# Optimization experiments

Hardware: AMD Instinct MI355X
Metric: run time of the kernel (lower is better)

Reference implementation:

```python
import jax, jax.numpy as jnp
import numpy as np

B, C, H, Wd = 4, 64, 64, 64


def setup_inputs() -> dict:
    key = jax.random.key(0)
    k1, k2, k3 = jax.random.split(key, 3)
    x = jax.random.normal(k1, (B, C, H, Wd), dtype=jnp.float32)
    W = jax.random.normal(k2, (C, C), dtype=jnp.float32) * (1.0 / np.sqrt(C))
    b = jax.random.normal(k3, (C,), dtype=jnp.float32) * 0.01
    return {"x": x, "W": W, "b": b}


def reference(x, W, b):
    Bz, Cz, Hz, Wz = x.shape
    N = Hz * Wz
    xf = x.reshape(Bz, Cz, N)                      # values [B,C,N]
    # shared 1x1 conv for queries and keys (same module instance in torch)
    qk = jnp.einsum('oc,bcn->bon', W, xf) + b[None, :, None]  # [B,C,N]
    # scores[b,n,m] = sum_c q[b,c,n] * k[b,c,m], scaled by 1/N
    scores = jnp.einsum('bcn,bcm->bnm', qk, qk) / N           # [B,N,N]
    attn = jax.nn.softmax(scores, axis=-1)                    # softmax over m
    # out[b,c,n] = sum_m values[b,c,m] * attn[b,n,m]
    out = jnp.einsum('bcm,bnm->bcn', xf, attn)
    return out.reshape(Bz, Cz, Hz, Wz)
```

## Files before the change

### kernel.cpp

```cpp
#include <hip/hip_runtime.h>
#include <hip/hip_bf16.h>

#define BATCH 4
#define NSP   4096

typedef __bf16 bf16x8v __attribute__((ext_vector_type(8)));
typedef __bf16 bf16x4v __attribute__((ext_vector_type(4)));
typedef float  floatx4 __attribute__((ext_vector_type(4)));

__global__ __launch_bounds__(256) void qk_kernel(const float* __restrict__ x,
                                                 const float* __restrict__ Wm,
                                                 const float* __restrict__ bias,
                                                 __bf16* __restrict__ qkT) {
    __shared__ __align__(16) __bf16 xT[64 * 72];

    const int t  = threadIdx.x;
    const int b  = blockIdx.x >> 6;
    const int n0 = (blockIdx.x & 63) << 6;

#pragma unroll
    for (int p = 0; p < 4; ++p) {
        const int c  = p * 16 + (t >> 4);
        const int n4 = (t & 15) * 4;
        const float4 v = *(const float4*)(x + (size_t)(b * 64 + c) * 4096 + n0 + n4);
        xT[(n4 + 0) * 72 + c] = (__bf16)(v.x * 0.015625f);
        xT[(n4 + 1) * 72 + c] = (__bf16)(v.y * 0.015625f);
        xT[(n4 + 2) * 72 + c] = (__bf16)(v.z * 0.015625f);
        xT[(n4 + 3) * 72 + c] = (__bf16)(v.w * 0.015625f);
    }
    __syncthreads();

    const int w = t >> 6, lane = t & 63, quad = lane >> 4, l16 = lane & 15;
    const bf16x8v a0 = *(const bf16x8v*)(xT + (w * 16 + l16) * 72 + quad * 8);
    const bf16x8v a1 = *(const bf16x8v*)(xT + (w * 16 + l16) * 72 + 32 + quad * 8);

    floatx4 acc[4];
#pragma unroll
    for (int ot = 0; ot < 4; ++ot) {
        const float* wr = Wm + (ot * 16 + l16) * 64;
        float4 wa = *(const float4*)(wr + quad * 8);
        float4 wb = *(const float4*)(wr + quad * 8 + 4);
        float4 wc = *(const float4*)(wr + 32 + quad * 8);
        float4 wd = *(const float4*)(wr + 32 + quad * 8 + 4);
        bf16x8v b0, b1;
        b0[0]=(__bf16)wa.x; b0[1]=(__bf16)wa.y; b0[2]=(__bf16)wa.z; b0[3]=(__bf16)wa.w;
        b0[4]=(__bf16)wb.x; b0[5]=(__bf16)wb.y; b0[6]=(__bf16)wb.z; b0[7]=(__bf16)wb.w;
        b1[0]=(__bf16)wc.x; b1[1]=(__bf16)wc.y; b1[2]=(__bf16)wc.z; b1[3]=(__bf16)wc.w;
        b1[4]=(__bf16)wd.x; b1[5]=(__bf16)wd.y; b1[6]=(__bf16)wd.z; b1[7]=(__bf16)wd.w;
        acc[ot] = floatx4{0.f, 0.f, 0.f, 0.f};
        acc[ot] = __builtin_amdgcn_mfma_f32_16x16x32_bf16(a0, b0, acc[ot], 0, 0, 0);
        acc[ot] = __builtin_amdgcn_mfma_f32_16x16x32_bf16(a1, b1, acc[ot], 0, 0, 0);
    }
    __syncthreads();

#pragma unroll
    for (int ot = 0; ot < 4; ++ot) {
        const float bo = bias[ot * 16 + l16] * 0.015625f;
#pragma unroll
        for (int r = 0; r < 4; ++r)
            xT[(w * 16 + quad * 4 + r) * 72 + ot * 16 + l16] = (__bf16)(acc[ot][r] + bo);
    }
    __syncthreads();

    const int n = t >> 2, seg = t & 3;
    __bf16* dst = qkT + (size_t)(b * 4096 + n0 + n) * 64 + seg * 16;
    *(bf16x8v*)dst       = *(const bf16x8v*)(xT + n * 72 + seg * 16);
    *(bf16x8v*)(dst + 8) = *(const bf16x8v*)(xT + n * 72 + seg * 16 + 8);
}

template<int SPLIT, int ITERS>
__global__ __launch_bounds__(256, 4) void attn_kernel(const float* __restrict__ x,
                                                      const __bf16* __restrict__ qkT,
                                                      __bf16* __restrict__ Opart,
                                                      float* __restrict__ Lpart) {
    __shared__ __align__(16) char smem[36864];
    __bf16* Klds = (__bf16*)smem;
    __bf16* Vlds = (__bf16*)(smem + 9216);
    __bf16* Plds = (__bf16*)(smem + 18432);
    float*  Olds = (float*)smem;

    const int t   = threadIdx.x;
    const int blk = blockIdx.x;
    const int xcd = blk & 7;
    const int b   = xcd >> 1;
    const int sub = ((blk >> 3) << 1) | (xcd & 1);
    const int qt  = sub / SPLIT;
    const int s   = sub % SPLIT;
    const int n0  = qt << 7;
    const int pblk = (b * 32 + qt) * SPLIT + s;

    const int w = t >> 6, lane = t & 63, quad = lane >> 4, l16 = lane & 15;

    bf16x8v fq[2][2];
#pragma unroll
    for (int qt2 = 0; qt2 < 2; ++qt2) {
        const __bf16* qrow = qkT + (size_t)(b * 4096 + n0 + w * 32 + qt2 * 16 + l16) * 64;
        fq[qt2][0] = *(const bf16x8v*)(qrow + quad * 8);
        fq[qt2][1] = *(const bf16x8v*)(qrow + 32 + quad * 8);
    }

    floatx4 oacc[2][4];
#pragma unroll
    for (int i = 0; i < 2; ++i)
#pragma unroll
        for (int j = 0; j < 4; ++j) oacc[i][j] = floatx4{0.f, 0.f, 0.f, 0.f};
    float rs[2] = {0.f, 0.f};

    for (int it = 0; it < ITERS; ++it) {
        const int m0 = s * (64 * ITERS) + (it << 6);
        __syncthreads();
#pragma unroll
        for (int i = 0; i < 2; ++i) {
            int idx = t + 256 * i;
            int row = idx >> 3, c8 = idx & 7;
            *(uint4*)(Klds + row * 72 + c8 * 8) =
                *(const uint4*)(qkT + (size_t)(b * 4096 + m0 + row) * 64 + c8 * 8);
        }
#pragma unroll
        for (int i = 0; i < 4; ++i) {
            int idx = t + 256 * i;
            int c = idx >> 4, f4 = idx & 15;
            const float4 v = *(const float4*)(x + (size_t)(b * 64 + c) * 4096 + m0 + f4 * 4);
            bf16x4v bv;
            bv[0] = (__bf16)v.x; bv[1] = (__bf16)v.y; bv[2] = (__bf16)v.z; bv[3] = (__bf16)v.w;
            *(bf16x4v*)(Vlds + c * 72 + f4 * 4) = bv;
        }
        __syncthreads();

#pragma unroll
        for (int mt = 0; mt < 4; ++mt) {
            const __bf16* kr = Klds + (mt * 16 + l16) * 72;
            bf16x8v ak0 = *(const bf16x8v*)(kr + quad * 8);
            bf16x8v ak1 = *(const bf16x8v*)(kr + 32 + quad * 8);
#pragma unroll
            for (int qt2 = 0; qt2 < 2; ++qt2) {
                floatx4 sT = {0.f, 0.f, 0.f, 0.f};
                sT = __builtin_amdgcn_mfma_f32_16x16x32_bf16(ak0, fq[qt2][0], sT, 0, 0, 0);
                sT = __builtin_amdgcn_mfma_f32_16x16x32_bf16(ak1, fq[qt2][1], sT, 0, 0, 0);
                float p0 = __expf(sT[0]), p1 = __expf(sT[1]);
                float p2 = __expf(sT[2]), p3 = __expf(sT[3]);
                rs[qt2] += (p0 + p1) + (p2 + p3);
                bf16x4v pv;
                pv[0] = (__bf16)p0; pv[1] = (__bf16)p1; pv[2] = (__bf16)p2; pv[3] = (__bf16)p3;
                *(bf16x4v*)(Plds + (w * 32 + qt2 * 16 + l16) * 72 + mt * 16 + quad * 4) = pv;
            }
        }

        bf16x8v ap[2][2];
#pragma unroll
        for (int qt2 = 0; qt2 < 2; ++qt2) {
            const __bf16* pr = Plds + (w * 32 + qt2 * 16 + l16) * 72;
            ap[qt2][0] = *(const bf16x8v*)(pr + quad * 8);
            ap[qt2][1] = *(const bf16x8v*)(pr + 32 + quad * 8);
        }
#pragma unroll
        for (int ct = 0; ct < 4; ++ct) {
            const __bf16* vr = Vlds + (ct * 16 + l16) * 72;
            bf16x8v bv0 = *(const bf16x8v*)(vr + quad * 8);
            bf16x8v bv1 = *(const bf16x8v*)(vr + 32 + quad * 8);
#pragma unroll
            for (int qt2 = 0; qt2 < 2; ++qt2) {
                oacc[qt2][ct] = __builtin_amdgcn_mfma_f32_16x16x32_bf16(ap[qt2][0], bv0, oacc[qt2][ct], 0, 0, 0);
                oacc[qt2][ct] = __builtin_amdgcn_mfma_f32_16x16x32_bf16(ap[qt2][1], bv1, oacc[qt2][ct], 0, 0, 0);
            }
        }
    }

#pragma unroll
    for (int qt2 = 0; qt2 < 2; ++qt2) {
        float v = rs[qt2];
        v += __shfl_xor(v, 16, 64);
        v += __shfl_xor(v, 32, 64);
        if (quad == 0)
            Lpart[(size_t)pblk * 128 + w * 32 + qt2 * 16 + l16] = v;
    }

    __syncthreads();

#pragma unroll
    for (int qt2 = 0; qt2 < 2; ++qt2)
#pragma unroll
        for (int ct = 0; ct < 4; ++ct)
#pragma unroll
            for (int r = 0; r < 4; ++r)
                Olds[(ct * 16 + l16) * 132 + w * 32 + qt2 * 16 + quad * 4 + r] = oacc[qt2][ct][r];
    __syncthreads();

    const int c = t >> 2, seg = t & 3;
#pragma unroll
    for (int i = 0; i < 4; ++i) {
        floatx4 v0 = *(const floatx4*)(Olds + c * 132 + seg * 32 + i * 8);
        floatx4 v1 = *(const floatx4*)(Olds + c * 132 + seg * 32 + i * 8 + 4);
        bf16x8v pk;
        pk[0]=(__bf16)v0[0]; pk[1]=(__bf16)v0[1]; pk[2]=(__bf16)v0[2]; pk[3]=(__bf16)v0[3];
        pk[4]=(__bf16)v1[0]; pk[5]=(__bf16)v1[1]; pk[6]=(__bf16)v1[2]; pk[7]=(__bf16)v1[3];
        *(bf16x8v*)(Opart + (size_t)pblk * 8192 + c * 128 + seg * 32 + i * 8) = pk;
    }
}

template<int SPLIT>
__global__ __launch_bounds__(256) void reduce_kernel(const __bf16* __restrict__ Opart,
                                                     const float* __restrict__ Lpart,
                                                     float* __restrict__ out) {
    const int blk = blockIdx.x;
    const int bq = blk >> 2, cq = blk & 3;
    const int b = bq >> 5, qt = bq & 31;
    const int t = threadIdx.x;
    const int c  = cq * 16 + (t >> 4);
    const int q8 = (t & 15) * 8;

    float l[8] = {0.f,0.f,0.f,0.f,0.f,0.f,0.f,0.f};
#pragma unroll
    for (int s = 0; s < SPLIT; ++s) {
        const float* lp = Lpart + ((size_t)bq * SPLIT + s) * 128 + q8;
        float4 u = *(const float4*)lp;
        float4 v = *(const float4*)(lp + 4);
        l[0]+=u.x; l[1]+=u.y; l[2]+=u.z; l[3]+=u.w;
        l[4]+=v.x; l[5]+=v.y; l[6]+=v.z; l[7]+=v.w;
    }
    float a[8] = {0.f,0.f,0.f,0.f,0.f,0.f,0.f,0.f};
#pragma unroll
    for (int s = 0; s < SPLIT; ++s) {
        bf16x8v v = *(const bf16x8v*)(Opart + ((size_t)bq * SPLIT + s) * 8192 + c * 128 + q8);
#pragma unroll
        for (int k = 0; k < 8; ++k) a[k] += (float)v[k];
    }
    float* op = out + (size_t)(b * 64 + c) * 4096 + qt * 128 + q8;
    float4 o0, o1;
    o0.x = a[0]/l[0]; o0.y = a[1]/l[1]; o0.z = a[2]/l[2]; o0.w = a[3]/l[3];
    o1.x = a[4]/l[4]; o1.y = a[5]/l[5]; o1.z = a[6]/l[6]; o1.w = a[7]/l[7];
    *(float4*)op       = o0;
    *(float4*)(op + 4) = o1;
}

extern "C" void kernel_launch(void* const* d_in, const int* in_sizes, int n_in,
                              void* d_out, int out_size, void* d_ws, size_t ws_size,
                              hipStream_t stream) {
    const float* x    = (const float*)d_in[0];
    const float* Wm   = (const float*)d_in[1];
    const float* bias = (const float*)d_in[2];
    float* out = (float*)d_out;

    char* ws = (char*)d_ws;
    __bf16* qkT = (__bf16*)ws;

    qk_kernel<<<BATCH * (NSP / 64), 256, 0, stream>>>(x, Wm, bias, qkT);

    const size_t QKT = 2097152;
    const size_t needBig = QKT + (size_t)1024 * 8192 * 2 + (size_t)1024 * 128 * 4;
    if (ws_size >= needBig) {
        __bf16* Opart = (__bf16*)(ws + QKT);
        float*  Lpart = (float*)(ws + QKT + (size_t)1024 * 8192 * 2);
        attn_kernel<8, 8><<<BATCH * 32 * 8, 256, 0, stream>>>(x, qkT, Opart, Lpart);
        reduce_kernel<8><<<512, 256, 0, stream>>>(Opart, Lpart, out);
    } else {
        __bf16* Opart = (__bf16*)(ws + QKT);
        float*  Lpart = (float*)(ws + QKT + (size_t)512 * 8192 * 2);
        attn_kernel<4, 16><<<BATCH * 32 * 4, 256, 0, stream>>>(x, qkT, Opart, Lpart);
        reduce_kernel<4><<<512, 256, 0, stream>>>(Opart, Lpart, out);
    }
}
```

Measured before the change: 101.2 us.

## Prefetch K/V into registers and keep P in registers via 16x16x16 MFMA

The attention loop now issues global loads for the next K/V tile into registers before computing on the current tile, so load latency can overlap the MFMA work. When the 16x16x16 bf16 MFMA builtin is available, the softmax probabilities stay in registers as B operands instead of going through LDS. The PV product is therefore transposed and the output staging layout changes to match. The reduce kernel computes reciprocal row sums once into shared memory and multiplies instead of dividing. These changes add register pressure, which could hurt occupancy at 4 blocks per CU, and use an MFMA with half the K depth.

```diff
diff --git a/kernel.cpp b/kernel.cpp
--- a/kernel.cpp
+++ b/kernel.cpp
@@ -7,6 +7,22 @@
 typedef __bf16 bf16x8v __attribute__((ext_vector_type(8)));
 typedef __bf16 bf16x4v __attribute__((ext_vector_type(4)));
 typedef float  floatx4 __attribute__((ext_vector_type(4)));
+typedef short  shortx4 __attribute__((ext_vector_type(4)));
+
+#if __has_builtin(__builtin_amdgcn_mfma_f32_16x16x16bf16_1k)
+#define HAVE_MFMA16 1
+static __device__ inline floatx4 mfma16(bf16x4v a, bf16x4v b, floatx4 c) {
+    return __builtin_amdgcn_mfma_f32_16x16x16bf16_1k(
+        __builtin_bit_cast(shortx4, a), __builtin_bit_cast(shortx4, b), c, 0, 0, 0);
+}
+#elif __has_builtin(__builtin_amdgcn_mfma_f32_16x16x16_bf16)
+#define HAVE_MFMA16 1
+static __device__ inline floatx4 mfma16(bf16x4v a, bf16x4v b, floatx4 c) {
+    return __builtin_amdgcn_mfma_f32_16x16x16_bf16(a, b, c, 0, 0, 0);
+}
+#else
+#define HAVE_MFMA16 0
+#endif
 
 __global__ __launch_bounds__(256) void qk_kernel(const float* __restrict__ x,
                                                  const float* __restrict__ Wm,
@@ -76,7 +92,9 @@
     __shared__ __align__(16) char smem[36864];
     __bf16* Klds = (__bf16*)smem;
     __bf16* Vlds = (__bf16*)(smem + 9216);
+#if !HAVE_MFMA16
     __bf16* Plds = (__bf16*)(smem + 18432);
+#endif
     float*  Olds = (float*)smem;
 
     const int t   = threadIdx.x;
@@ -106,27 +124,53 @@
         for (int j = 0; j < 4; ++j) oacc[i][j] = floatx4{0.f, 0.f, 0.f, 0.f};
     float rs[2] = {0.f, 0.f};
 
-    for (int it = 0; it < ITERS; ++it) {
-        const int m0 = s * (64 * ITERS) + (it << 6);
-        __syncthreads();
+    uint4  kpre[2];
+    float4 vpre[4];
+    {
+        const int m0 = s * (64 * ITERS);
 #pragma unroll
         for (int i = 0; i < 2; ++i) {
             int idx = t + 256 * i;
-            int row = idx >> 3, c8 = idx & 7;
-            *(uint4*)(Klds + row * 72 + c8 * 8) =
-                *(const uint4*)(qkT + (size_t)(b * 4096 + m0 + row) * 64 + c8 * 8);
+            kpre[i] = *(const uint4*)(qkT + (size_t)(b * 4096 + m0 + (idx >> 3)) * 64 + (idx & 7) * 8);
         }
 #pragma unroll
         for (int i = 0; i < 4; ++i) {
             int idx = t + 256 * i;
-            int c = idx >> 4, f4 = idx & 15;
-            const float4 v = *(const float4*)(x + (size_t)(b * 64 + c) * 4096 + m0 + f4 * 4);
+            vpre[i] = *(const float4*)(x + (size_t)(b * 64 + (idx >> 4)) * 4096 + m0 + (idx & 15) * 4);
+        }
+    }
+
+    for (int it = 0; it < ITERS; ++it) {
+        __syncthreads();
+#pragma unroll
+        for (int i = 0; i < 2; ++i) {
+            int idx = t + 256 * i;
+            *(uint4*)(Klds + (idx >> 3) * 72 + (idx & 7) * 8) = kpre[i];
+        }
+#pragma unroll
+        for (int i = 0; i < 4; ++i) {
+            int idx = t + 256 * i;
             bf16x4v bv;
-            bv[0] = (__bf16)v.x; bv[1] = (__bf16)v.y; bv[2] = (__bf16)v.z; bv[3] = (__bf16)v.w;
-            *(bf16x4v*)(Vlds + c * 72 + f4 * 4) = bv;
+            bv[0] = (__bf16)vpre[i].x; bv[1] = (__bf16)vpre[i].y;
+            bv[2] = (__bf16)vpre[i].z; bv[3] = (__bf16)vpre[i].w;
+            *(bf16x4v*)(Vlds + (idx >> 4) * 72 + (idx & 15) * 4) = bv;
         }
         __syncthreads();
-
+        if (it + 1 < ITERS) {
+            const int m1 = s * (64 * ITERS) + ((it + 1) << 6);
+#pragma unroll
+            for (int i = 0; i < 2; ++i) {
+                int idx = t + 256 * i;
+                kpre[i] = *(const uint4*)(qkT + (size_t)(b * 4096 + m1 + (idx >> 3)) * 64 + (idx & 7) * 8);
+            }
+#pragma unroll
+            for (int i = 0; i < 4; ++i) {
+                int idx = t + 256 * i;
+                vpre[i] = *(const float4*)(x + (size_t)(b * 64 + (idx >> 4)) * 4096 + m1 + (idx & 15) * 4);
+            }
+        }
+
+        bf16x4v pf[4][2];
 #pragma unroll
         for (int mt = 0; mt < 4; ++mt) {
             const __bf16* kr = Klds + (mt * 16 + l16) * 72;
@@ -142,10 +186,28 @@
                 rs[qt2] += (p0 + p1) + (p2 + p3);
                 bf16x4v pv;
                 pv[0] = (__bf16)p0; pv[1] = (__bf16)p1; pv[2] = (__bf16)p2; pv[3] = (__bf16)p3;
+#if HAVE_MFMA16
+                pf[mt][qt2] = pv;
+#else
                 *(bf16x4v*)(Plds + (w * 32 + qt2 * 16 + l16) * 72 + mt * 16 + quad * 4) = pv;
-            }
-        }
-
+#endif
+            }
+        }
+
+#if HAVE_MFMA16
+#pragma unroll
+        for (int ct = 0; ct < 4; ++ct) {
+            const __bf16* vb = Vlds + (ct * 16 + l16) * 72;
+#pragma unroll
+            for (int mt = 0; mt < 4; ++mt) {
+                bf16x4v av = *(const bf16x4v*)(vb + mt * 16 + quad * 4);
+#pragma unroll
+                for (int qt2 = 0; qt2 < 2; ++qt2)
+                    oacc[qt2][ct] = mfma16(av, pf[mt][qt2], oacc[qt2][ct]);
+            }
+        }
+#else
+        (void)pf;
         bf16x8v ap[2][2];
 #pragma unroll
         for (int qt2 = 0; qt2 < 2; ++qt2) {
@@ -164,6 +226,7 @@
                 oacc[qt2][ct] = __builtin_amdgcn_mfma_f32_16x16x32_bf16(ap[qt2][1], bv1, oacc[qt2][ct], 0, 0, 0);
             }
         }
+#endif
     }
 
 #pragma unroll
@@ -177,6 +240,15 @@
 
     __syncthreads();
 
+#if HAVE_MFMA16
+#pragma unroll
+    for (int qt2 = 0; qt2 < 2; ++qt2)
+#pragma unroll
+        for (int ct = 0; ct < 4; ++ct)
+#pragma unroll
+            for (int r = 0; r < 4; ++r)
+                Olds[(ct * 16 + quad * 4 + r) * 132 + w * 32 + qt2 * 16 + l16] = oacc[qt2][ct][r];
+#else
 #pragma unroll
     for (int qt2 = 0; qt2 < 2; ++qt2)
 #pragma unroll
@@ -184,6 +256,7 @@
 #pragma unroll
             for (int r = 0; r < 4; ++r)
                 Olds[(ct * 16 + l16) * 132 + w * 32 + qt2 * 16 + quad * 4 + r] = oacc[qt2][ct][r];
+#endif
     __syncthreads();
 
     const int c = t >> 2, seg = t & 3;
@@ -202,22 +275,24 @@
 __global__ __launch_bounds__(256) void reduce_kernel(const __bf16* __restrict__ Opart,
                                                      const float* __restrict__ Lpart,
                                                      float* __restrict__ out) {
+    __shared__ float linv[128];
     const int blk = blockIdx.x;
     const int bq = blk >> 2, cq = blk & 3;
     const int b = bq >> 5, qt = bq & 31;
     const int t = threadIdx.x;
+
+    if (t < 128) {
+        float sl = 0.f;
+#pragma unroll
+        for (int s = 0; s < SPLIT; ++s)
+            sl += Lpart[((size_t)bq * SPLIT + s) * 128 + t];
+        linv[t] = 1.0f / sl;
+    }
+    __syncthreads();
+
     const int c  = cq * 16 + (t >> 4);
     const int q8 = (t & 15) * 8;
 
-    float l[8] = {0.f,0.f,0.f,0.f,0.f,0.f,0.f,0.f};
-#pragma unroll
-    for (int s = 0; s < SPLIT; ++s) {
-        const float* lp = Lpart + ((size_t)bq * SPLIT + s) * 128 + q8;
-        float4 u = *(const float4*)lp;
-        float4 v = *(const float4*)(lp + 4);
-        l[0]+=u.x; l[1]+=u.y; l[2]+=u.z; l[3]+=u.w;
-        l[4]+=v.x; l[5]+=v.y; l[6]+=v.z; l[7]+=v.w;
-    }
     float a[8] = {0.f,0.f,0.f,0.f,0.f,0.f,0.f,0.f};
 #pragma unroll
     for (int s = 0; s < SPLIT; ++s) {
@@ -227,8 +302,8 @@
     }
     float* op = out + (size_t)(b * 64 + c) * 4096 + qt * 128 + q8;
     float4 o0, o1;
-    o0.x = a[0]/l[0]; o0.y = a[1]/l[1]; o0.z = a[2]/l[2]; o0.w = a[3]/l[3];
-    o1.x = a[4]/l[4]; o1.y = a[5]/l[5]; o1.z = a[6]/l[6]; o1.w = a[7]/l[7];
+    o0.x = a[0]*linv[q8+0]; o0.y = a[1]*linv[q8+1]; o0.z = a[2]*linv[q8+2]; o0.w = a[3]*linv[q8+3];
+    o1.x = a[4]*linv[q8+4]; o1.y = a[5]*linv[q8+5]; o1.z = a[6]*linv[q8+6]; o1.w = a[7]*linv[q8+7];
     *(float4*)op       = o0;
     *(float4*)(op + 4) = o1;
 }
```

After: 105.1 us. 1.04x slower.

## Double-buffer K/V tiles with register prefetch and keep P in registers

Applied to the files above, without the earlier changes.

The attention loop now prefetches the next K and V tiles into registers and stores them into alternating LDS buffers, which removes one barrier per iteration and overlaps global loads with compute. The P matrix is no longer staged through LDS. The second MFMA stage is recomputed as O^T using K=16 bf16 MFMAs that consume the softmax accumulator fragments directly, with a permuted V layout and transposed output write. The reduce kernel computes the reciprocal of the row sums once in shared memory instead of doing per-element divides. In exchange it uses more registers and issues twice as many smaller MFMAs.

```diff
diff --git a/kernel.cpp b/kernel.cpp
--- a/kernel.cpp
+++ b/kernel.cpp
@@ -7,6 +7,24 @@
 typedef __bf16 bf16x8v __attribute__((ext_vector_type(8)));
 typedef __bf16 bf16x4v __attribute__((ext_vector_type(4)));
 typedef float  floatx4 __attribute__((ext_vector_type(4)));
+typedef short  shortx4 __attribute__((ext_vector_type(4)));
+
+#if defined(__HIP_DEVICE_COMPILE__)
+#  if __has_builtin(__builtin_amdgcn_mfma_f32_16x16x16bf16_1k)
+static __device__ inline floatx4 mfma16(bf16x4v a, bf16x4v b, floatx4 c) {
+    return __builtin_amdgcn_mfma_f32_16x16x16bf16_1k(
+        __builtin_bit_cast(shortx4, a), __builtin_bit_cast(shortx4, b), c, 0, 0, 0);
+}
+#  elif __has_builtin(__builtin_amdgcn_mfma_f32_16x16x16_bf16)
+static __device__ inline floatx4 mfma16(bf16x4v a, bf16x4v b, floatx4 c) {
+    return __builtin_amdgcn_mfma_f32_16x16x16_bf16(a, b, c, 0, 0, 0);
+}
+#  else
+#    error "gfx950 device pass should have a K=16 bf16 mfma builtin"
+#  endif
+#else
+static __device__ inline floatx4 mfma16(bf16x4v, bf16x4v, floatx4 c) { return c; }
+#endif
 
 __global__ __launch_bounds__(256) void qk_kernel(const float* __restrict__ x,
                                                  const float* __restrict__ Wm,
@@ -68,16 +86,15 @@
     *(bf16x8v*)(dst + 8) = *(const bf16x8v*)(xT + n * 72 + seg * 16 + 8);
 }
 
+#define BUFB 18432
+
 template<int SPLIT, int ITERS>
 __global__ __launch_bounds__(256, 4) void attn_kernel(const float* __restrict__ x,
                                                       const __bf16* __restrict__ qkT,
                                                       __bf16* __restrict__ Opart,
                                                       float* __restrict__ Lpart) {
     __shared__ __align__(16) char smem[36864];
-    __bf16* Klds = (__bf16*)smem;
-    __bf16* Vlds = (__bf16*)(smem + 9216);
-    __bf16* Plds = (__bf16*)(smem + 18432);
-    float*  Olds = (float*)smem;
+    float* Olds = (float*)smem;
 
     const int t   = threadIdx.x;
     const int blk = blockIdx.x;
@@ -106,30 +123,51 @@
         for (int j = 0; j < 4; ++j) oacc[i][j] = floatx4{0.f, 0.f, 0.f, 0.f};
     float rs[2] = {0.f, 0.f};
 
+    const int krow = t >> 3, kc8 = (t & 7) * 8;
+    const int vc   = t >> 4, vk  = t & 15;
+    const int vj   = (vk & 3) * 16 + (vk >> 2) * 4;
+    const __bf16* kgp = qkT + (size_t)b * 4096 * 64 + (size_t)s * (64 * ITERS) * 64;
+    const float*  vgp = x + (size_t)b * 64 * 4096 + s * (64 * ITERS);
+
+    uint4  kpre[2];
+    float4 vpre[4];
+#pragma unroll
+    for (int i = 0; i < 2; ++i)
+        kpre[i] = *(const uint4*)(kgp + (size_t)(krow + i * 32) * 64 + kc8);
+#pragma unroll
+    for (int i = 0; i < 4; ++i)
+        vpre[i] = *(const float4*)(vgp + (size_t)(vc + i * 16) * 4096 + vk * 4);
+
     for (int it = 0; it < ITERS; ++it) {
-        const int m0 = s * (64 * ITERS) + (it << 6);
-        __syncthreads();
-#pragma unroll
-        for (int i = 0; i < 2; ++i) {
-            int idx = t + 256 * i;
-            int row = idx >> 3, c8 = idx & 7;
-            *(uint4*)(Klds + row * 72 + c8 * 8) =
-                *(const uint4*)(qkT + (size_t)(b * 4096 + m0 + row) * 64 + c8 * 8);
-        }
+        __bf16* Kb = (__bf16*)(smem + (it & 1) * BUFB);
+        __bf16* Vb = (__bf16*)(smem + (it & 1) * BUFB + 9216);
+
+#pragma unroll
+        for (int i = 0; i < 2; ++i)
+            *(uint4*)(Kb + (krow + i * 32) * 72 + kc8) = kpre[i];
 #pragma unroll
         for (int i = 0; i < 4; ++i) {
-            int idx = t + 256 * i;
-            int c = idx >> 4, f4 = idx & 15;
-            const float4 v = *(const float4*)(x + (size_t)(b * 64 + c) * 4096 + m0 + f4 * 4);
             bf16x4v bv;
-            bv[0] = (__bf16)v.x; bv[1] = (__bf16)v.y; bv[2] = (__bf16)v.z; bv[3] = (__bf16)v.w;
-            *(bf16x4v*)(Vlds + c * 72 + f4 * 4) = bv;
+            bv[0] = (__bf16)vpre[i].x; bv[1] = (__bf16)vpre[i].y;
+            bv[2] = (__bf16)vpre[i].z; bv[3] = (__bf16)vpre[i].w;
+            *(bf16x4v*)(Vb + (vc + i * 16) * 72 + vj) = bv;
         }
         __syncthreads();
 
+        if (it + 1 < ITERS) {
+            const int m1 = (it + 1) << 6;
+#pragma unroll
+            for (int i = 0; i < 2; ++i)
+                kpre[i] = *(const uint4*)(kgp + (size_t)(m1 + krow + i * 32) * 64 + kc8);
+#pragma unroll
+            for (int i = 0; i < 4; ++i)
+                vpre[i] = *(const float4*)(vgp + (size_t)(vc + i * 16) * 4096 + m1 + vk * 4);
+        }
+
+        bf16x4v pf[4][2];
 #pragma unroll
         for (int mt = 0; mt < 4; ++mt) {
-            const __bf16* kr = Klds + (mt * 16 + l16) * 72;
+            const __bf16* kr = Kb + (mt * 16 + l16) * 72;
             bf16x8v ak0 = *(const bf16x8v*)(kr + quad * 8);
             bf16x8v ak1 = *(const bf16x8v*)(kr + 32 + quad * 8);
 #pragma unroll
@@ -142,26 +180,25 @@
                 rs[qt2] += (p0 + p1) + (p2 + p3);
                 bf16x4v pv;
                 pv[0] = (__bf16)p0; pv[1] = (__bf16)p1; pv[2] = (__bf16)p2; pv[3] = (__bf16)p3;
-                *(bf16x4v*)(Plds + (w * 32 + qt2 * 16 + l16) * 72 + mt * 16 + quad * 4) = pv;
+                pf[mt][qt2] = pv;
             }
         }
 
-        bf16x8v ap[2][2];
-#pragma unroll
-        for (int qt2 = 0; qt2 < 2; ++qt2) {
-            const __bf16* pr = Plds + (w * 32 + qt2 * 16 + l16) * 72;
-            ap[qt2][0] = *(const bf16x8v*)(pr + quad * 8);
-            ap[qt2][1] = *(const bf16x8v*)(pr + 32 + quad * 8);
-        }
 #pragma unroll
         for (int ct = 0; ct < 4; ++ct) {
-            const __bf16* vr = Vlds + (ct * 16 + l16) * 72;
-            bf16x8v bv0 = *(const bf16x8v*)(vr + quad * 8);
-            bf16x8v bv1 = *(const bf16x8v*)(vr + 32 + quad * 8);
+            const __bf16* vb = Vb + (ct * 16 + l16) * 72 + quad * 16;
+            bf16x8v v01 = *(const bf16x8v*)vb;
+            bf16x8v v23 = *(const bf16x8v*)(vb + 8);
+            bf16x4v av0 = {v01[0], v01[1], v01[2], v01[3]};
+            bf16x4v av1 = {v01[4], v01[5], v01[6], v01[7]};
+            bf16x4v av2 = {v23[0], v23[1], v23[2], v23[3]};
+            bf16x4v av3 = {v23[4], v23[5], v23[6], v23[7]};
 #pragma unroll
             for (int qt2 = 0; qt2 < 2; ++qt2) {
-                oacc[qt2][ct] = __builtin_amdgcn_mfma_f32_16x16x32_bf16(ap[qt2][0], bv0, oacc[qt2][ct], 0, 0, 0);
-                oacc[qt2][ct] = __builtin_amdgcn_mfma_f32_16x16x32_bf16(ap[qt2][1], bv1, oacc[qt2][ct], 0, 0, 0);
+                oacc[qt2][ct] = mfma16(av0, pf[0][qt2], oacc[qt2][ct]);
+                oacc[qt2][ct] = mfma16(av1, pf[1][qt2], oacc[qt2][ct]);
+                oacc[qt2][ct] = mfma16(av2, pf[2][qt2], oacc[qt2][ct]);
+                oacc[qt2][ct] = mfma16(av3, pf[3][qt2], oacc[qt2][ct]);
             }
         }
     }
@@ -183,7 +220,7 @@
         for (int ct = 0; ct < 4; ++ct)
 #pragma unroll
             for (int r = 0; r < 4; ++r)
-                Olds[(ct * 16 + l16) * 132 + w * 32 + qt2 * 16 + quad * 4 + r] = oacc[qt2][ct][r];
+                Olds[(ct * 16 + quad * 4 + r) * 132 + w * 32 + qt2 * 16 + l16] = oacc[qt2][ct][r];
     __syncthreads();
 
     const int c = t >> 2, seg = t & 3;
@@ -202,22 +239,24 @@
 __global__ __launch_bounds__(256) void reduce_kernel(const __bf16* __restrict__ Opart,
                                                      const float* __restrict__ Lpart,
                                                      float* __restrict__ out) {
+    __shared__ float linv[128];
     const int blk = blockIdx.x;
     const int bq = blk >> 2, cq = blk & 3;
     const int b = bq >> 5, qt = bq & 31;
     const int t = threadIdx.x;
+
+    if (t < 128) {
+        float sl = 0.f;
+#pragma unroll
+        for (int s = 0; s < SPLIT; ++s)
+            sl += Lpart[((size_t)bq * SPLIT + s) * 128 + t];
+        linv[t] = 1.0f / sl;
+    }
+    __syncthreads();
+
     const int c  = cq * 16 + (t >> 4);
     const int q8 = (t & 15) * 8;
 
-    float l[8] = {0.f,0.f,0.f,0.f,0.f,0.f,0.f,0.f};
-#pragma unroll
-    for (int s = 0; s < SPLIT; ++s) {
-        const float* lp = Lpart + ((size_t)bq * SPLIT + s) * 128 + q8;
-        float4 u = *(const float4*)lp;
-        float4 v = *(const float4*)(lp + 4);
-        l[0]+=u.x; l[1]+=u.y; l[2]+=u.z; l[3]+=u.w;
-        l[4]+=v.x; l[5]+=v.y; l[6]+=v.z; l[7]+=v.w;
-    }
     float a[8] = {0.f,0.f,0.f,0.f,0.f,0.f,0.f,0.f};
 #pragma unroll
     for (int s = 0; s < SPLIT; ++s) {
@@ -227,8 +266,8 @@
     }
     float* op = out + (size_t)(b * 64 + c) * 4096 + qt * 128 + q8;
     float4 o0, o1;
-    o0.x = a[0]/l[0]; o0.y = a[1]/l[1]; o0.z = a[2]/l[2]; o0.w = a[3]/l[3];
-    o1.x = a[4]/l[4]; o1.y = a[5]/l[5]; o1.z = a[6]/l[6]; o1.w = a[7]/l[7];
+    o0.x = a[0]*linv[q8+0]; o0.y = a[1]*linv[q8+1]; o0.z = a[2]*linv[q8+2]; o0.w = a[3]*linv[q8+3];
+    o1.x = a[4]*linv[q8+4]; o1.y = a[5]*linv[q8+5]; o1.z = a[6]*linv[q8+6]; o1.w = a[7]*linv[q8+7];
     *(float4*)op       = o0;
     *(float4*)(op + 4) = o1;
 }
```

Result: no change. 101.8 us (+0.6%).
